# Kernel tuning notes

Hardware: AMD Instinct MI355X
Metric: run time of the kernel (lower is better)

Reference implementation:

```python
import jax, jax.numpy as jnp
import numpy as np

H, E, V, F, P, B = 512, 512, 10000, 1280, 196, 32
SOS = 1

def setup_inputs() -> dict:
    key = jax.random.key(0)
    ks = jax.random.split(key, 24)
    s = 0.02
    return {
        "feature_outputs": jax.random.normal(ks[0], (B, P, F), jnp.float32),
        "caption": jax.random.randint(ks[1], (B, 80), 0, V),
        "max_caption": 80,
        "embedding": jax.random.normal(ks[2], (V, E), jnp.float32) * s,
        "W1_w": jax.random.normal(ks[3], (H, H), jnp.float32) * s,
        "W1_b": jnp.full((H,), 0.01, jnp.float32),
        "W2_w": jax.random.normal(ks[4], (H, F), jnp.float32) * s,
        "W2_b": jnp.full((H,), 0.01, jnp.float32),
        "Va_w": jax.random.normal(ks[5], (1, H), jnp.float32) * s,
        "Va_b": jnp.full((1,), 0.01, jnp.float32),
        "lstm_Wih": jax.random.normal(ks[6], (4 * H, E + F), jnp.float32) * s,
        "lstm_Whh": jax.random.normal(ks[7], (4 * H, H), jnp.float32) * s,
        "lstm_bih": jnp.zeros((4 * H,), jnp.float32),
        "lstm_bhh": jnp.zeros((4 * H,), jnp.float32),
        "out_w": jax.random.normal(ks[8], (V, H), jnp.float32) * s,
        "out_b": jnp.full((V,), 0.01, jnp.float32),
        "init_h_w": jax.random.normal(ks[9], (H, F), jnp.float32) * s,
        "init_h_b": jnp.full((H,), 0.01, jnp.float32),
        "init_c_w": jax.random.normal(ks[10], (H, F), jnp.float32) * s,
        "init_c_b": jnp.full((H,), 0.01, jnp.float32),
        "gate_w": jax.random.normal(ks[11], (F, H), jnp.float32) * s,
        "gate_b": jnp.full((F,), 0.01, jnp.float32),
    }


def reference(feature_outputs, caption, max_caption, embedding,
              W1_w, W1_b, W2_w, W2_b, Va_w, Va_b,
              lstm_Wih, lstm_Whh, lstm_bih, lstm_bhh,
              out_w, out_b, init_h_w, init_h_b, init_c_w, init_c_b,
              gate_w, gate_b):
    steps = int(max_caption)
    bsz = caption.shape[0]
    mean_enc = feature_outputs.mean(axis=1)                       # [B,F]
    h0 = mean_enc @ init_h_w.T + init_h_b                         # [B,H]
    c0 = mean_enc @ init_c_w.T + init_c_b                         # [B,H]
    # W2(keys) is constant across steps -> hoist out of the loop
    enc_proj = jnp.einsum('bpf,hf->bph', feature_outputs, W2_w) + W2_b  # [B,P,H]
    inp0 = jnp.broadcast_to(embedding[SOS], (bsz, embedding.shape[1]))  # [B,E]

    def step(carry, _):
        h, c, inp = carry
        # Bahdanau attention
        hid = h @ W1_w.T + W1_b                                   # [B,H]
        scores = (jax.nn.relu(hid[:, None, :] + enc_proj) @ Va_w[0] + Va_b[0])  # [B,P]
        weights = jax.nn.softmax(scores, axis=1)
        context = jnp.einsum('bpf,bp->bf', feature_outputs, weights)  # [B,F]
        gate = jax.nn.sigmoid(h @ gate_w.T + gate_b)              # [B,F]
        context = context * gate
        # LSTMCell (torch gate order: i, f, g, o)
        x = jnp.concatenate([inp, context], axis=1)               # [B,E+F]
        gates = x @ lstm_Wih.T + lstm_bih + h @ lstm_Whh.T + lstm_bhh
        i_g, f_g, g_g, o_g = jnp.split(gates, 4, axis=1)
        c_new = jax.nn.sigmoid(f_g) * c + jax.nn.sigmoid(i_g) * jnp.tanh(g_g)
        h_new = jax.nn.sigmoid(o_g) * jnp.tanh(c_new)
        logits = h_new @ out_w.T + out_b                          # [B,V] (dropout = eval identity)
        nxt = embedding[jnp.argmax(logits, axis=-1)]              # greedy decode
        return (h_new, c_new, nxt), (logits, weights)

    (h, c, _), (outs, attns) = jax.lax.scan(step, (h0, c0, inp0), None, length=steps)
    decoder_outputs = jnp.transpose(outs, (1, 0, 2))              # [B,T,V]
    attentions = jnp.transpose(attns, (1, 0, 2))                  # [B,T,P]
    return decoder_outputs, (h, c), attentions
```

## Files before the change

### kernel.cpp

```cpp
#include <hip/hip_runtime.h>
#include <hip/hip_cooperative_groups.h>
#include <math.h>

#define RI __restrict__

namespace {

constexpr int Hn=512, En=512, Vn=10000, Fn=1280, Pn=196, Bn=32, Tn=80;
constexpr int G4 = 2048, KX = 1792;
constexpr int NCAT = 13888;
constexpr int NVT = 157;
constexpr int J_GATE = 512, J_XP = 1792, J_LOG = 3840;
constexpr int NBLK = 256;
constexpr int XROW = 140;

constexpr long O_ENC  = 0;
constexpr long O_W2T  = O_ENC  + (long)Bn*Pn*Hn;
constexpr long O_WCAT = O_W2T  + (long)Fn*Hn;
constexpr long O_WIHT = O_WCAT + (long)Hn*NCAT;
constexpr long O_C    = O_WIHT + (long)KX*G4;
constexpr long O_HT   = O_C    + (long)Bn*Hn;
constexpr long O_HID  = O_HT   + (long)Hn*Bn;
constexpr long O_GT   = O_HID  + (long)Bn*Hn;
constexpr long O_XPT  = O_GT   + (long)Bn*Fn;
constexpr long O_XT   = O_XPT  + (long)G4*Bn;
constexpr long O_PMV  = O_XT   + (long)Bn*KX;
constexpr long O_PMI  = O_PMV  + (long)Bn*NVT;
constexpr long O_SVAL = O_PMI  + (long)Bn*NVT;
constexpr long O_SEL  = O_SVAL + (long)Bn*Pn;
constexpr long O_CNT  = O_SEL  + 64;
constexpr long O_IHCT  = O_ENC;
constexpr long O_MEANT = O_ENC + (long)Fn*1024;

__device__ __forceinline__ float sigm(float x){ return 1.0f/(1.0f+expf(-x)); }
__device__ __forceinline__ void fma4(float4& a, const float4 x, const float w){
  a.x += w*x.x; a.y += w*x.y; a.z += w*x.z; a.w += w*x.w;
}
__device__ __forceinline__ float ldc(const float* p){
  return __hip_atomic_load(p, __ATOMIC_RELAXED, __HIP_MEMORY_SCOPE_AGENT);
}
__device__ __forceinline__ void stc(float* p, float v){
  __hip_atomic_store(p, v, __ATOMIC_RELAXED, __HIP_MEMORY_SCOPE_AGENT);
}
__device__ __forceinline__ int ldci(const int* p){
  return __hip_atomic_load(p, __ATOMIC_RELAXED, __HIP_MEMORY_SCOPE_AGENT);
}
__device__ __forceinline__ void stci(int* p, int v){
  __hip_atomic_store(p, v, __ATOMIC_RELAXED, __HIP_MEMORY_SCOPE_AGENT);
}
__device__ __forceinline__ float2 ldc2(const float* p){
  union { unsigned long long u; float2 f; } c;
  c.u = __hip_atomic_load((const unsigned long long*)p,
                          __ATOMIC_RELAXED, __HIP_MEMORY_SCOPE_AGENT);
  return c.f;
}

__device__ __forceinline__ void gbar(unsigned* cnt, unsigned target){
  __syncthreads();
  if (threadIdx.x == 0){
    __hip_atomic_fetch_add(cnt, 1u, __ATOMIC_RELAXED, __HIP_MEMORY_SCOPE_AGENT);
    while (__hip_atomic_load(cnt, __ATOMIC_RELAXED, __HIP_MEMORY_SCOPE_AGENT) < target)
      __builtin_amdgcn_s_sleep(2);
  }
  __syncthreads();
}

__global__ __launch_bounds__(256) void k_tr_s(const float* RI src, float* RI dst,
                                              int R, int C, int S){
  __shared__ float t[32][33];
  int tc0 = blockIdx.x*32, tr0 = blockIdx.y*32;
  int lx = threadIdx.x & 31, ly = threadIdx.x >> 5;
  for (int i = ly; i < 32; i += 8){
    int r = tr0 + i, c = tc0 + lx;
    t[i][lx] = (r < R && c < C) ? src[(long)r*C + c] : 0.f;
  }
  __syncthreads();
  for (int i = ly; i < 32; i += 8){
    int c = tc0 + i, r = tr0 + lx;
    if (c < C && r < R) dst[(long)c*S + r] = t[lx][i];
  }
}

__global__ __launch_bounds__(256) void k_tr_wih(const float* RI src, float* RI ws){
  __shared__ float t[32][33];
  int tk0 = blockIdx.x*32, tj0 = blockIdx.y*32;
  int lx = threadIdx.x & 31, ly = threadIdx.x >> 5;
  for (int i = ly; i < 32; i += 8){
    int j = tj0 + i, k = tk0 + lx;
    t[i][lx] = src[(long)j*KX + k];
  }
  __syncthreads();
  for (int i = ly; i < 32; i += 8){
    int k = tk0 + i, j = tj0 + lx;
    int pc = ((j & 511) << 2) | (j >> 9);
    ws[O_WIHT + ((long)(pc >> 3)*KX + k)*8 + (pc & 7)] = t[lx][i];
  }
}

__global__ __launch_bounds__(256) void k_mean(const float* RI feat, float* RI ws){
  int blk = blockIdx.x;
  int b = blk / 5, ft = blk % 5;
  int f = ft*256 + threadIdx.x;
  float s = 0.f;
  const float* fp = feat + (long)b*Pn*Fn + f;
  for (int p = 0; p < Pn; ++p) s += fp[(long)p*Fn];
  ws[O_MEANT + (long)f*Bn + b] = s * (1.0f/Pn);
}

__global__ __launch_bounds__(512) void k_h0c0(const float* RI ihb, const float* RI icb,
                                              float* RI ws){
  int tid = threadIdx.x;
  int jl = tid & 63, bq = tid >> 6;
  int j = blockIdx.x*64 + jl;
  const float* wp = ws + O_IHCT + j;
  const float* xp = ws + O_MEANT + bq*4;
  float4 acc = make_float4(0,0,0,0);
  for (int k = 0; k < Fn; ++k){
    float w = wp[(long)k*1024];
    float4 x = *(const float4*)(xp + (long)k*Bn);
    fma4(acc, x, w);
  }
  float va[4] = {acc.x, acc.y, acc.z, acc.w};
  if (j < Hn){
    float bias = ihb[j];
    #pragma unroll
    for (int m = 0; m < 4; ++m)
      ws[O_HT + (long)j*Bn + (bq*4+m)] = va[m] + bias;
  } else {
    int j2 = j - Hn;
    float bias = icb[j2];
    #pragma unroll
    for (int m = 0; m < 4; ++m)
      ws[O_C + (long)(bq*4+m)*Hn + j2] = va[m] + bias;
  }
}

__global__ __launch_bounds__(512) void k_encproj(const float* RI feat, const float* RI w2b,
                                                 float* RI ws){
  __shared__ __align__(16) float xs[64*65];
  const int blk = blockIdx.x;
  const int rt = blk >> 2, ct = blk & 3;
  const int r0 = rt*64, j0 = ct*128;
  const int tid = threadIdx.x;
  const int jq = tid & 31, rg = tid >> 5;
  const int rw = tid >> 3, kc = (tid & 7)*8;
  const float* w2t = ws + O_W2T + j0 + jq*4;
  float4 a0 = make_float4(0,0,0,0), a1 = a0, a2 = a0, a3 = a0;
  for (int k0 = 0; k0 < Fn; k0 += 64){
    __syncthreads();
    {
      const float* fp = feat + (long)(r0+rw)*Fn + k0 + kc;
      float4 v0 = *(const float4*)(fp);
      float4 v1 = *(const float4*)(fp + 4);
      float* xr = xs + rw*65 + kc;
      xr[0]=v0.x; xr[1]=v0.y; xr[2]=v0.z; xr[3]=v0.w;
      xr[4]=v1.x; xr[5]=v1.y; xr[6]=v1.z; xr[7]=v1.w;
    }
    __syncthreads();
    #pragma unroll 4
    for (int kk = 0; kk < 64; ++kk){
      float4 w = *(const float4*)(w2t + (long)(k0+kk)*Hn);
      const float* xp = xs + (rg*4)*65 + kk;
      fma4(a0, w, xp[0]);
      fma4(a1, w, xp[65]);
      fma4(a2, w, xp[130]);
      fma4(a3, w, xp[195]);
    }
  }
  float4 b4 = *(const float4*)(w2b + j0 + jq*4);
  float4 out[4] = {a0,a1,a2,a3};
  #pragma unroll
  for (int m = 0; m < 4; ++m){
    long r = r0 + rg*4 + m;
    float4 o = out[m];
    o.x += b4.x; o.y += b4.y; o.z += b4.z; o.w += b4.w;
    *(float4*)(ws + O_ENC + r*Hn + j0 + jq*4) = o;
  }
}

__global__ __launch_bounds__(512) void k_decode(
    const float* RI feat, const float* RI emb, const float* RI vaw, const float* RI vab,
    const float* RI w1b, const float* RI gb, const float* RI bih, const float* RI bhh,
    const float* RI outb, float* RI ws, float* RI dout)
{
  __shared__ __align__(16) float wlds[32768];
  __shared__ __align__(16) float sbuf[4608];
  const int blk = blockIdx.x, tid = threadIdx.x;
  const int jl = tid & 63, bq = tid >> 6;
  unsigned* cnt = (unsigned*)(ws + O_CNT);

  if (blk < 217){
    const float* wg = ws + O_WCAT + blk*64;
    for (int idx = tid; idx < 512*64; idx += 512){
      int k = idx >> 6, j = idx & 63;
      wlds[idx] = wg[(long)k*NCAT + j];
    }
  }
  __syncthreads();

  for (int t = 0; t <= Tn; ++t){
    bool p1act;
    if (t == Tn)      p1act = (blk >= 60 && blk < 217);
    else if (t == 0)  p1act = (blk < 60);
    else              p1act = (blk < 217);
    if (p1act){
      float4 acc = make_float4(0,0,0,0);
      float2 pre0 = ldc2(ws + O_HT + tid*2);
      float2 pre1 = ldc2(ws + O_HT + 1024 + tid*2);
      for (int c8 = 0; c8 < 8; ++c8){
        __syncthreads();
        *(float2*)(sbuf + tid*2) = pre0;
        *(float2*)(sbuf + 1024 + tid*2) = pre1;
        __syncthreads();
        if (c8 < 7){
          pre0 = ldc2(ws + O_HT + (long)(c8+1)*2048 + tid*2);
          pre1 = ldc2(ws + O_HT + (long)(c8+1)*2048 + 1024 + tid*2);
        }
        #pragma unroll 8
        for (int kk = 0; kk < 64; ++kk){
          float w = wlds[(long)(c8*64 + kk)*64 + jl];
          float4 x = *(const float4*)(sbuf + kk*32 + bq*4);
          fma4(acc, x, w);
        }
      }
      __syncthreads();
      const int j = blk*64 + jl;
      if (blk < 8){
        float bias = w1b[j];
        stc(ws + O_HID + (long)(bq*4+0)*Hn + j, acc.x + bias);
        stc(ws + O_HID + (long)(bq*4+1)*Hn + j, acc.y + bias);
        stc(ws + O_HID + (long)(bq*4+2)*Hn + j, acc.z + bias);
        stc(ws + O_HID + (long)(bq*4+3)*Hn + j, acc.w + bias);
      } else if (blk < 28){
        int f = j - J_GATE;
        float bias = gb[f];
        stc(ws + O_GT + (long)(bq*4+0)*Fn + f, sigm(acc.x + bias));
        stc(ws + O_GT + (long)(bq*4+1)*Fn + f, sigm(acc.y + bias));
        stc(ws + O_GT + (long)(bq*4+2)*Fn + f, sigm(acc.z + bias));
        stc(ws + O_GT + (long)(bq*4+3)*Fn + f, sigm(acc.w + bias));
      } else if (blk < 60){
        int j2 = j - J_XP;
        float bias = bih[j2] + bhh[j2];
        sbuf[jl*33 + bq*4+0] = acc.x + bias;
        sbuf[jl*33 + bq*4+1] = acc.y + bias;
        sbuf[jl*33 + bq*4+2] = acc.z + bias;
        sbuf[jl*33 + bq*4+3] = acc.w + bias;
        __syncthreads();
        #pragma unroll
        for (int r = 0; r < 4; ++r){
          int idx = r*512 + tid;
          int row = idx >> 5, b = idx & 31;
          int j2r = (blk-28)*64 + row;
          int pc = ((j2r & 511) << 2) | (j2r >> 9);
          stc(ws + O_XPT + (long)pc*Bn + b, sbuf[row*33 + b]);
        }
      } else {
        int v = j - J_LOG;
        float lv[4];
        if (v < Vn){
          float bias = outb[v];
          lv[0]=acc.x+bias; lv[1]=acc.y+bias; lv[2]=acc.z+bias; lv[3]=acc.w+bias;
          #pragma unroll
          for (int m = 0; m < 4; ++m)
            dout[((long)(bq*4+m)*Tn + (t-1))*Vn + v] = lv[m];
        } else {
          lv[0]=lv[1]=lv[2]=lv[3]=-1e30f;
        }
        int tile = blk - 60;
        #pragma unroll
        for (int m = 0; m < 4; ++m){
          float bv = lv[m]; int bi = v;
          #pragma unroll
          for (int off = 32; off; off >>= 1){
            float ov = __shfl_down(bv, off, 64);
            int   oi = __shfl_down(bi, off, 64);
            if (ov > bv || (ov == bv && oi < bi)){ bv = ov; bi = oi; }
          }
          if (jl == 0){
            int b = bq*4 + m;
            stc (ws + O_PMV + (long)b*NVT + tile, bv);
            stci((int*)(ws + O_PMI) + (long)b*NVT + tile, bi);
          }
        }
      }
    }
    gbar(cnt, 256u*(t+1));
    if (t == Tn) break;

    if (blk < 224){
      const int b = blk & 31, part = blk >> 5;
      float* hid_s = sbuf;
      float* va_s  = sbuf + 512;
      float* sv    = sbuf + 1024;
      hid_s[tid] = ldc(ws + O_HID + (long)b*Hn + tid);
      va_s[tid]  = vaw[tid];
      __syncthreads();
      const int w = tid >> 6, l = tid & 63;
      const int p0 = part*28;
      const float* eb = ws + O_ENC + (long)b*Pn*Hn;
      #pragma unroll 2
      for (int p = p0 + w; p < p0 + 28; p += 8){
        const float* er = eb + (long)p*Hn;
        float4 e0 = *(const float4*)(er + l*4);
        float4 e1 = *(const float4*)(er + 256 + l*4);
        float4 h0 = *(const float4*)(hid_s + l*4);
        float4 h1 = *(const float4*)(hid_s + 256 + l*4);
        float4 v0 = *(const float4*)(va_s + l*4);
        float4 v1 = *(const float4*)(va_s + 256 + l*4);
        float s = fmaxf(h0.x+e0.x,0.f)*v0.x + fmaxf(h0.y+e0.y,0.f)*v0.y
                + fmaxf(h0.z+e0.z,0.f)*v0.z + fmaxf(h0.w+e0.w,0.f)*v0.w
                + fmaxf(h1.x+e1.x,0.f)*v1.x + fmaxf(h1.y+e1.y,0.f)*v1.y
                + fmaxf(h1.z+e1.z,0.f)*v1.z + fmaxf(h1.w+e1.w,0.f)*v1.w;
        #pragma unroll
        for (int off = 32; off; off >>= 1) s += __shfl_down(s, off, 64);
        if (l == 0) sv[p - p0] = s + vab[0];
      }
      __syncthreads();
      if (tid < 28) stc(ws + O_SVAL + (long)b*Pn + p0 + tid, sv[tid]);
    } else {
      const int b = blk - 224;
      if (t == 0){
        if (tid == 0) stci((int*)(ws + O_SEL) + b, 1);
      } else if (tid < 64){
        float bv = -1e30f; int bi = 0x7fffffff;
        for (int q = tid; q < NVT; q += 64){
          float cv = ldc(ws + O_PMV + (long)b*NVT + q);
          if (cv > bv){ bv = cv; bi = ldci((const int*)(ws + O_PMI) + (long)b*NVT + q); }
        }
        #pragma unroll
        for (int off = 32; off; off >>= 1){
          float ov = __shfl_down(bv, off, 64);
          int   oi = __shfl_down(bi, off, 64);
          if (ov > bv || (ov == bv && oi < bi)){ bv = ov; bi = oi; }
        }
        if (tid == 0) stci((int*)(ws + O_SEL) + b, bi);
      }
    }
    gbar(cnt + 32, 256u*(t+1));

    {
      const int b = blk & 31, fr = blk >> 5;
      const int f0 = fr*160;
      float* svl = sbuf;
      float* wts = sbuf + 208;
      if (tid < Pn) svl[tid] = ldc(ws + O_SVAL + (long)b*Pn + tid);
      if (tid == 0) ((int*)sbuf)[450] = ldci((const int*)(ws + O_SEL) + b);
      __syncthreads();
      if (tid < 64){
        float m = -1e30f;
        for (int p = tid; p < Pn; p += 64) m = fmaxf(m, svl[p]);
        #pragma unroll
        for (int off = 32; off; off >>= 1) m = fmaxf(m, __shfl_xor(m, off, 64));
        float sm = 0.f;
        for (int p = tid; p < Pn; p += 64) sm += expf(svl[p] - m);
        #pragma unroll
        for (int off = 32; off; off >>= 1) sm += __shfl_xor(sm, off, 64);
        if (tid == 0){ sbuf[448] = m; sbuf[449] = 1.0f/sm; }
      }
      __syncthreads();
      if (tid < Pn){
        float wv = expf(svl[tid] - sbuf[448]) * sbuf[449];
        wts[tid] = wv;
        if (fr == 0)
          dout[(long)Bn*Tn*Vn + 2L*Bn*Hn + ((long)b*Tn + t)*Pn + tid] = wv;
      }
      __syncthreads();
      const int pp = tid / 160, fl = tid - pp*160;
      float a = 0.f;
      if (tid < 480){
        const int p0 = pp*66, pn = (pp == 2) ? 64 : 66;
        const float* fp = feat + ((long)b*Pn + p0)*Fn + f0 + fl;
        const float* wl = wts + p0;
        float s0=0,s1=0,s2=0,s3=0,s4=0,s5=0,s6=0,s7=0;
        int p = 0;
        for (; p + 8 <= pn; p += 8){
          s0 += wl[p+0]*__builtin_nontemporal_load(fp + (long)(p+0)*Fn);
          s1 += wl[p+1]*__builtin_nontemporal_load(fp + (long)(p+1)*Fn);
          s2 += wl[p+2]*__builtin_nontemporal_load(fp + (long)(p+2)*Fn);
          s3 += wl[p+3]*__builtin_nontemporal_load(fp + (long)(p+3)*Fn);
          s4 += wl[p+4]*__builtin_nontemporal_load(fp + (long)(p+4)*Fn);
          s5 += wl[p+5]*__builtin_nontemporal_load(fp + (long)(p+5)*Fn);
          s6 += wl[p+6]*__builtin_nontemporal_load(fp + (long)(p+6)*Fn);
          s7 += wl[p+7]*__builtin_nontemporal_load(fp + (long)(p+7)*Fn);
        }
        for (; p < pn; ++p) s0 += wl[p]*__builtin_nontemporal_load(fp + (long)p*Fn);
        a = ((s0+s1)+(s2+s3)) + ((s4+s5)+(s6+s7));
        if (pp > 0) sbuf[512 + (pp-1)*160 + fl] = a;
      }
      __syncthreads();
      if (tid < 160){
        float tot = a + sbuf[512 + tid] + sbuf[672 + tid];
        int f = f0 + tid;
        tot *= ldc(ws + O_GT + (long)b*Fn + f);
        stc(ws + O_XT + (long)b*KX + En + f, tot);
      }
      if (fr == 0){
        int row = ((int*)sbuf)[450];
        stc(ws + O_XT + (long)b*KX + tid, emb[(long)row*En + tid]);
      }
    }
    gbar(cnt + 64, 256u*(t+1));

    {
      const int c = tid & 7, ks = tid >> 3;
      const int pc0 = blk*8;
      const float* wg = ws + O_WIHT + (long)blk*KX*8;
      float4 acc4[8];
      #pragma unroll
      for (int q = 0; q < 8; ++q) acc4[q] = make_float4(0,0,0,0);
      float2 pre[4];
      #pragma unroll
      for (int r = 0; r < 4; ++r){
        int flat = r*1024 + tid*2;
        pre[r] = ldc2(ws + O_XT + (long)(flat >> 7)*KX + (flat & 127));
      }
      for (int ch = 0; ch < 14; ++ch){
        __syncthreads();
        #pragma unroll
        for (int r = 0; r < 4; ++r){
          int flat = r*1024 + tid*2;
          int kl = flat & 127, b = flat >> 7;
          int sc = kl + ((kl >> 5) << 2);
          float* xd = sbuf + b*XROW;
          xd[sc] = pre[r].x; xd[sc+1] = pre[r].y;
        }
        __syncthreads();
        if (ch < 13){
          long k0n = (long)(ch+1)*128;
          #pragma unroll
          for (int r = 0; r < 4; ++r){
            int flat = r*1024 + tid*2;
            pre[r] = ldc2(ws + O_XT + (long)(flat >> 7)*KX + k0n + (flat & 127));
          }
        }
        const long kg0 = (long)ch*128;
        #pragma unroll
        for (int kk = 0; kk < 2; ++kk){
          int kl = ks*2 + kk;
          float w = wg[(kg0 + kl)*8 + c];
          int cs = kl + ((kl >> 5) << 2);
          const float* xq = sbuf + cs;
          #pragma unroll
          for (int q = 0; q < 8; ++q){
            const float* xb = xq + (q*4)*XROW;
            acc4[q].x += w * xb[0];
            acc4[q].y += w * xb[XROW];
            acc4[q].z += w * xb[2*XROW];
            acc4[q].w += w * xb[3*XROW];
          }
        }
      }
      #pragma unroll
      for (int off = 8; off <= 32; off <<= 1){
        #pragma unroll
        for (int q = 0; q < 8; ++q){
          acc4[q].x += __shfl_xor(acc4[q].x, off, 64);
          acc4[q].y += __shfl_xor(acc4[q].y, off, 64);
          acc4[q].z += __shfl_xor(acc4[q].z, off, 64);
          acc4[q].w += __shfl_xor(acc4[q].w, off, 64);
        }
      }
      __syncthreads();
      const int wv = tid >> 6, lane = tid & 63;
      if (lane < 8){
        float* rb = sbuf + (wv*8 + lane)*32;
        #pragma unroll
        for (int q = 0; q < 8; ++q) *(float4*)(rb + q*4) = acc4[q];
      }
      __syncthreads();
      if (tid < 256){
        int cc = tid >> 5, b = tid & 31;
        float s = 0.f;
        #pragma unroll
        for (int w2 = 0; w2 < 8; ++w2) s += sbuf[(w2*8 + cc)*32 + b];
        s += ldc(ws + O_XPT + (long)(pc0 + cc)*Bn + b);
        sbuf[2048 + cc*32 + b] = s;
      }
      __syncthreads();
      if (tid < 64){
        int il = tid >> 5, b = tid & 31;
        int i = blk*2 + il;
        float gi  = sbuf[2048 + (il*4+0)*32 + b];
        float gf  = sbuf[2048 + (il*4+1)*32 + b];
        float gg2 = sbuf[2048 + (il*4+2)*32 + b];
        float go  = sbuf[2048 + (il*4+3)*32 + b];
        float c_ = ws[O_C + (long)b*Hn + i];
        float cn = sigm(gf)*c_ + sigm(gi)*tanhf(gg2);
        float hn = sigm(go)*tanhf(cn);
        ws[O_C + (long)b*Hn + i] = cn;
        stc(ws + O_HT + (long)i*Bn + b, hn);
        if (t == Tn-1){
          dout[(long)Bn*Tn*Vn + (long)b*Hn + i] = hn;
          dout[(long)Bn*Tn*Vn + (long)Bn*Hn + (long)b*Hn + i] = cn;
        }
      }
    }
    gbar(cnt + 96, 256u*(t+1));
  }
}

}

extern "C" void kernel_launch(void* const* d_in, const int* in_sizes, int n_in,
                              void* d_out, int out_size, void* d_ws, size_t ws_size,
                              hipStream_t stream)
{
  (void)in_sizes; (void)n_in; (void)out_size; (void)ws_size;
  const float* feat = (const float*)d_in[0];
  const float* emb  = (const float*)d_in[3];
  const float* w1w  = (const float*)d_in[4];
  const float* w1b  = (const float*)d_in[5];
  const float* w2w  = (const float*)d_in[6];
  const float* w2b  = (const float*)d_in[7];
  const float* vaw  = (const float*)d_in[8];
  const float* vab  = (const float*)d_in[9];
  const float* wih  = (const float*)d_in[10];
  const float* whh  = (const float*)d_in[11];
  const float* bih  = (const float*)d_in[12];
  const float* bhh  = (const float*)d_in[13];
  const float* outw = (const float*)d_in[14];
  const float* outb = (const float*)d_in[15];
  const float* ihw  = (const float*)d_in[16];
  const float* ihb  = (const float*)d_in[17];
  const float* icw  = (const float*)d_in[18];
  const float* icb  = (const float*)d_in[19];
  const float* gw   = (const float*)d_in[20];
  const float* gb   = (const float*)d_in[21];
  float* ws  = (float*)d_ws;
  float* out = (float*)d_out;

  hipMemsetAsync((char*)d_ws + O_CNT*sizeof(float), 0, 512, stream);

  k_tr_s<<<dim3(40,16),  256, 0, stream>>>(ihw,  ws + O_IHCT,       Hn, Fn, 1024);
  k_tr_s<<<dim3(40,16),  256, 0, stream>>>(icw,  ws + O_IHCT + 512, Hn, Fn, 1024);
  k_mean<<<160, 256, 0, stream>>>(feat, ws);
  k_h0c0<<<16, 512, 0, stream>>>(ihb, icb, ws);
  k_tr_s<<<dim3(16,16),  256, 0, stream>>>(w1w,  ws + O_WCAT,          Hn, Hn, NCAT);
  k_tr_s<<<dim3(16,40),  256, 0, stream>>>(gw,   ws + O_WCAT + J_GATE, Fn, Hn, NCAT);
  k_tr_s<<<dim3(16,64),  256, 0, stream>>>(whh,  ws + O_WCAT + J_XP,   G4, Hn, NCAT);
  k_tr_s<<<dim3(16,313), 256, 0, stream>>>(outw, ws + O_WCAT + J_LOG,  Vn, Hn, NCAT);
  k_tr_wih<<<dim3(56,64), 256, 0, stream>>>(wih, ws);
  k_tr_s<<<dim3(40,16),  256, 0, stream>>>(w2w,  ws + O_W2T,           Hn, Fn, Hn);
  k_encproj<<<392, 512, 0, stream>>>(feat, w2b, ws);

  void* kargs[] = { (void*)&feat, (void*)&emb, (void*)&vaw, (void*)&vab,
                    (void*)&w1b, (void*)&gb, (void*)&bih, (void*)&bhh,
                    (void*)&outb, (void*)&ws, (void*)&out };
  hipLaunchCooperativeKernel((const void*)k_decode, dim3(NBLK), dim3(512),
                             kargs, 0, stream);
}
```

Before: 6.401 ms.

## Replace grid-wide barriers with per-role dataflow counters in decode loop

The four full-grid barriers per timestep are replaced by fine-grained counters, one per producer role (hidden, gate, xproj, logits, per-batch scores and selection, x-transposes, h). Each phase now waits only on the specific data it consumes. This lets blocks run ahead and overlap stages, for example attention starting as soon as the W1 hidden projection is done. Feature loads in the context reduction also switch from nontemporal to normal cached loads. The risk is memory-ordering hazards with relaxed atomics and more polling traffic on the counters.

New measurement: 5.624 ms. 12.1% less time.

```diff
diff --git a/kernel.cpp b/kernel.cpp
--- a/kernel.cpp
+++ b/kernel.cpp
@@ -54,13 +54,24 @@
                           __ATOMIC_RELAXED, __HIP_MEMORY_SCOPE_AGENT);
   return c.f;
 }
-
-__device__ __forceinline__ void gbar(unsigned* cnt, unsigned target){
+__device__ __forceinline__ unsigned ldcu(const unsigned* p){
+  return __hip_atomic_load(p, __ATOMIC_RELAXED, __HIP_MEMORY_SCOPE_AGENT);
+}
+__device__ __forceinline__ void incc(unsigned* p){
+  __hip_atomic_fetch_add(p, 1u, __ATOMIC_RELAXED, __HIP_MEMORY_SCOPE_AGENT);
+}
+
+__device__ __forceinline__ void w1(const unsigned* a, unsigned ta){
+  if (threadIdx.x == 0){
+    while (ldcu(a) < ta) __builtin_amdgcn_s_sleep(2);
+  }
   __syncthreads();
+}
+__device__ __forceinline__ void w3(const unsigned* a, unsigned ta,
+                                   const unsigned* b, unsigned tb,
+                                   const unsigned* c, unsigned tc){
   if (threadIdx.x == 0){
-    __hip_atomic_fetch_add(cnt, 1u, __ATOMIC_RELAXED, __HIP_MEMORY_SCOPE_AGENT);
-    while (__hip_atomic_load(cnt, __ATOMIC_RELAXED, __HIP_MEMORY_SCOPE_AGENT) < target)
-      __builtin_amdgcn_s_sleep(2);
+    while (ldcu(a) < ta || ldcu(b) < tb || ldcu(c) < tc) __builtin_amdgcn_s_sleep(2);
   }
   __syncthreads();
 }
@@ -188,6 +199,15 @@
   const int blk = blockIdx.x, tid = threadIdx.x;
   const int jl = tid & 63, bq = tid >> 6;
   unsigned* cnt = (unsigned*)(ws + O_CNT);
+  unsigned* C_H   = cnt + 0;
+  unsigned* C_P1  = cnt + 32;
+  unsigned* C_HID = cnt + 64;
+  unsigned* C_GT  = cnt + 96;
+  unsigned* C_XP  = cnt + 128;
+  unsigned* C_LOG = cnt + 160;
+  unsigned* C_XT  = cnt + 192;
+  #define C_SC(b)  (cnt + 256 + (b)*8)
+  #define C_SEL(b) (cnt + 512 + (b)*8)
 
   if (blk < 217){
     const float* wg = ws + O_WCAT + blk*64;
@@ -199,96 +219,102 @@
   __syncthreads();
 
   for (int t = 0; t <= Tn; ++t){
-    bool p1act;
-    if (t == Tn)      p1act = (blk >= 60 && blk < 217);
-    else if (t == 0)  p1act = (blk < 60);
-    else              p1act = (blk < 217);
-    if (p1act){
-      float4 acc = make_float4(0,0,0,0);
-      float2 pre0 = ldc2(ws + O_HT + tid*2);
-      float2 pre1 = ldc2(ws + O_HT + 1024 + tid*2);
-      for (int c8 = 0; c8 < 8; ++c8){
+    if (blk < 217){
+      if (t > 0) w1(C_H, 256u*t);
+      bool p1act = (t == Tn) ? (blk >= 60) : !(t == 0 && blk >= 60);
+      if (p1act){
+        float4 acc = make_float4(0,0,0,0);
+        float2 pre0 = ldc2(ws + O_HT + tid*2);
+        float2 pre1 = ldc2(ws + O_HT + 1024 + tid*2);
+        for (int c8 = 0; c8 < 8; ++c8){
+          __syncthreads();
+          *(float2*)(sbuf + tid*2) = pre0;
+          *(float2*)(sbuf + 1024 + tid*2) = pre1;
+          __syncthreads();
+          if (c8 < 7){
+            pre0 = ldc2(ws + O_HT + (long)(c8+1)*2048 + tid*2);
+            pre1 = ldc2(ws + O_HT + (long)(c8+1)*2048 + 1024 + tid*2);
+          }
+          #pragma unroll 8
+          for (int kk = 0; kk < 64; ++kk){
+            float w = wlds[(long)(c8*64 + kk)*64 + jl];
+            float4 x = *(const float4*)(sbuf + kk*32 + bq*4);
+            fma4(acc, x, w);
+          }
+        }
         __syncthreads();
-        *(float2*)(sbuf + tid*2) = pre0;
-        *(float2*)(sbuf + 1024 + tid*2) = pre1;
-        __syncthreads();
-        if (c8 < 7){
-          pre0 = ldc2(ws + O_HT + (long)(c8+1)*2048 + tid*2);
-          pre1 = ldc2(ws + O_HT + (long)(c8+1)*2048 + 1024 + tid*2);
-        }
-        #pragma unroll 8
-        for (int kk = 0; kk < 64; ++kk){
-          float w = wlds[(long)(c8*64 + kk)*64 + jl];
-          float4 x = *(const float4*)(sbuf + kk*32 + bq*4);
-          fma4(acc, x, w);
-        }
-      }
-      __syncthreads();
-      const int j = blk*64 + jl;
-      if (blk < 8){
-        float bias = w1b[j];
-        stc(ws + O_HID + (long)(bq*4+0)*Hn + j, acc.x + bias);
-        stc(ws + O_HID + (long)(bq*4+1)*Hn + j, acc.y + bias);
-        stc(ws + O_HID + (long)(bq*4+2)*Hn + j, acc.z + bias);
-        stc(ws + O_HID + (long)(bq*4+3)*Hn + j, acc.w + bias);
-      } else if (blk < 28){
-        int f = j - J_GATE;
-        float bias = gb[f];
-        stc(ws + O_GT + (long)(bq*4+0)*Fn + f, sigm(acc.x + bias));
-        stc(ws + O_GT + (long)(bq*4+1)*Fn + f, sigm(acc.y + bias));
-        stc(ws + O_GT + (long)(bq*4+2)*Fn + f, sigm(acc.z + bias));
-        stc(ws + O_GT + (long)(bq*4+3)*Fn + f, sigm(acc.w + bias));
-      } else if (blk < 60){
-        int j2 = j - J_XP;
-        float bias = bih[j2] + bhh[j2];
-        sbuf[jl*33 + bq*4+0] = acc.x + bias;
-        sbuf[jl*33 + bq*4+1] = acc.y + bias;
-        sbuf[jl*33 + bq*4+2] = acc.z + bias;
-        sbuf[jl*33 + bq*4+3] = acc.w + bias;
-        __syncthreads();
-        #pragma unroll
-        for (int r = 0; r < 4; ++r){
-          int idx = r*512 + tid;
-          int row = idx >> 5, b = idx & 31;
-          int j2r = (blk-28)*64 + row;
-          int pc = ((j2r & 511) << 2) | (j2r >> 9);
-          stc(ws + O_XPT + (long)pc*Bn + b, sbuf[row*33 + b]);
-        }
-      } else {
-        int v = j - J_LOG;
-        float lv[4];
-        if (v < Vn){
-          float bias = outb[v];
-          lv[0]=acc.x+bias; lv[1]=acc.y+bias; lv[2]=acc.z+bias; lv[3]=acc.w+bias;
+        const int j = blk*64 + jl;
+        if (blk < 8){
+          float bias = w1b[j];
+          stc(ws + O_HID + (long)(bq*4+0)*Hn + j, acc.x + bias);
+          stc(ws + O_HID + (long)(bq*4+1)*Hn + j, acc.y + bias);
+          stc(ws + O_HID + (long)(bq*4+2)*Hn + j, acc.z + bias);
+          stc(ws + O_HID + (long)(bq*4+3)*Hn + j, acc.w + bias);
+        } else if (blk < 28){
+          int f = j - J_GATE;
+          float bias = gb[f];
+          stc(ws + O_GT + (long)(bq*4+0)*Fn + f, sigm(acc.x + bias));
+          stc(ws + O_GT + (long)(bq*4+1)*Fn + f, sigm(acc.y + bias));
+          stc(ws + O_GT + (long)(bq*4+2)*Fn + f, sigm(acc.z + bias));
+          stc(ws + O_GT + (long)(bq*4+3)*Fn + f, sigm(acc.w + bias));
+        } else if (blk < 60){
+          int j2 = j - J_XP;
+          float bias = bih[j2] + bhh[j2];
+          sbuf[jl*33 + bq*4+0] = acc.x + bias;
+          sbuf[jl*33 + bq*4+1] = acc.y + bias;
+          sbuf[jl*33 + bq*4+2] = acc.z + bias;
+          sbuf[jl*33 + bq*4+3] = acc.w + bias;
+          __syncthreads();
           #pragma unroll
-          for (int m = 0; m < 4; ++m)
-            dout[((long)(bq*4+m)*Tn + (t-1))*Vn + v] = lv[m];
+          for (int r = 0; r < 4; ++r){
+            int idx = r*512 + tid;
+            int row = idx >> 5, b = idx & 31;
+            int j2r = (blk-28)*64 + row;
+            int pc = ((j2r & 511) << 2) | (j2r >> 9);
+            stc(ws + O_XPT + (long)pc*Bn + b, sbuf[row*33 + b]);
+          }
         } else {
-          lv[0]=lv[1]=lv[2]=lv[3]=-1e30f;
-        }
-        int tile = blk - 60;
-        #pragma unroll
-        for (int m = 0; m < 4; ++m){
-          float bv = lv[m]; int bi = v;
+          int v = j - J_LOG;
+          float lv[4];
+          if (v < Vn){
+            float bias = outb[v];
+            lv[0]=acc.x+bias; lv[1]=acc.y+bias; lv[2]=acc.z+bias; lv[3]=acc.w+bias;
+            #pragma unroll
+            for (int m = 0; m < 4; ++m)
+              dout[((long)(bq*4+m)*Tn + (t-1))*Vn + v] = lv[m];
+          } else {
+            lv[0]=lv[1]=lv[2]=lv[3]=-1e30f;
+          }
+          int tile = blk - 60;
           #pragma unroll
-          for (int off = 32; off; off >>= 1){
-            float ov = __shfl_down(bv, off, 64);
-            int   oi = __shfl_down(bi, off, 64);
-            if (ov > bv || (ov == bv && oi < bi)){ bv = ov; bi = oi; }
-          }
-          if (jl == 0){
-            int b = bq*4 + m;
-            stc (ws + O_PMV + (long)b*NVT + tile, bv);
-            stci((int*)(ws + O_PMI) + (long)b*NVT + tile, bi);
-          }
-        }
-      }
-    }
-    gbar(cnt, 256u*(t+1));
+          for (int m = 0; m < 4; ++m){
+            float bv = lv[m]; int bi = v;
+            #pragma unroll
+            for (int off = 32; off; off >>= 1){
+              float ov = __shfl_down(bv, off, 64);
+              int   oi = __shfl_down(bi, off, 64);
+              if (ov > bv || (ov == bv && oi < bi)){ bv = ov; bi = oi; }
+            }
+            if (jl == 0){
+              int b = bq*4 + m;
+              stc (ws + O_PMV + (long)b*NVT + tile, bv);
+              stci((int*)(ws + O_PMI) + (long)b*NVT + tile, bi);
+            }
+          }
+        }
+      }
+      __syncthreads();
+      if (tid == 0){
+        unsigned* role = (blk < 8) ? C_HID : (blk < 28) ? C_GT
+                       : (blk < 60) ? C_XP : C_LOG;
+        incc(role); incc(C_P1);
+      }
+    }
     if (t == Tn) break;
 
     if (blk < 224){
       const int b = blk & 31, part = blk >> 5;
+      w1(C_HID, 8u*(t+1));
       float* hid_s = sbuf;
       float* va_s  = sbuf + 512;
       float* sv    = sbuf + 1024;
@@ -317,8 +343,11 @@
       }
       __syncthreads();
       if (tid < 28) stc(ws + O_SVAL + (long)b*Pn + p0 + tid, sv[tid]);
+      __syncthreads();
+      if (tid == 0) incc(C_SC(b));
     } else {
       const int b = blk - 224;
+      w1(C_LOG, 157u*(t+1));
       if (t == 0){
         if (tid == 0) stci((int*)(ws + O_SEL) + b, 1);
       } else if (tid < 64){
@@ -335,12 +364,14 @@
         }
         if (tid == 0) stci((int*)(ws + O_SEL) + b, bi);
       }
-    }
-    gbar(cnt + 32, 256u*(t+1));
+      __syncthreads();
+      if (tid == 0) incc(C_SEL(b));
+    }
 
     {
       const int b = blk & 31, fr = blk >> 5;
       const int f0 = fr*160;
+      w3(C_SC(b), 7u*(t+1), C_SEL(b), (unsigned)(t+1), C_GT, 20u*(t+1));
       float* svl = sbuf;
       float* wts = sbuf + 208;
       if (tid < Pn) svl[tid] = ldc(ws + O_SVAL + (long)b*Pn + tid);
@@ -374,16 +405,16 @@
         float s0=0,s1=0,s2=0,s3=0,s4=0,s5=0,s6=0,s7=0;
         int p = 0;
         for (; p + 8 <= pn; p += 8){
-          s0 += wl[p+0]*__builtin_nontemporal_load(fp + (long)(p+0)*Fn);
-          s1 += wl[p+1]*__builtin_nontemporal_load(fp + (long)(p+1)*Fn);
-          s2 += wl[p+2]*__builtin_nontemporal_load(fp + (long)(p+2)*Fn);
-          s3 += wl[p+3]*__builtin_nontemporal_load(fp + (long)(p+3)*Fn);
-          s4 += wl[p+4]*__builtin_nontemporal_load(fp + (long)(p+4)*Fn);
-          s5 += wl[p+5]*__builtin_nontemporal_load(fp + (long)(p+5)*Fn);
-          s6 += wl[p+6]*__builtin_nontemporal_load(fp + (long)(p+6)*Fn);
-          s7 += wl[p+7]*__builtin_nontemporal_load(fp + (long)(p+7)*Fn);
-        }
-        for (; p < pn; ++p) s0 += wl[p]*__builtin_nontemporal_load(fp + (long)p*Fn);
+          s0 += wl[p+0]*fp[(long)(p+0)*Fn];
+          s1 += wl[p+1]*fp[(long)(p+1)*Fn];
+          s2 += wl[p+2]*fp[(long)(p+2)*Fn];
+          s3 += wl[p+3]*fp[(long)(p+3)*Fn];
+          s4 += wl[p+4]*fp[(long)(p+4)*Fn];
+          s5 += wl[p+5]*fp[(long)(p+5)*Fn];
+          s6 += wl[p+6]*fp[(long)(p+6)*Fn];
+          s7 += wl[p+7]*fp[(long)(p+7)*Fn];
+        }
+        for (; p < pn; ++p) s0 += wl[p]*fp[(long)p*Fn];
         a = ((s0+s1)+(s2+s3)) + ((s4+s5)+(s6+s7));
         if (pp > 0) sbuf[512 + (pp-1)*160 + fl] = a;
       }
@@ -398,10 +429,12 @@
         int row = ((int*)sbuf)[450];
         stc(ws + O_XT + (long)b*KX + tid, emb[(long)row*En + tid]);
       }
-    }
-    gbar(cnt + 64, 256u*(t+1));
+      __syncthreads();
+      if (tid == 0) incc(C_XT);
+    }
 
     {
+      w3(C_XT, 256u*(t+1), C_XP, 32u*(t+1), C_P1, 217u*(t+1));
       const int c = tid & 7, ks = tid >> 3;
       const int pc0 = blk*8;
       const float* wg = ws + O_WIHT + (long)blk*KX*8;
@@ -494,9 +527,12 @@
           dout[(long)Bn*Tn*Vn + (long)Bn*Hn + (long)b*Hn + i] = cn;
         }
       }
-    }
-    gbar(cnt + 96, 256u*(t+1));
-  }
+      __syncthreads();
+      if (tid == 0) incc(C_H);
+    }
+  }
+  #undef C_SC
+  #undef C_SEL
 }
 
 }
@@ -529,7 +565,7 @@
   float* ws  = (float*)d_ws;
   float* out = (float*)d_out;
 
-  hipMemsetAsync((char*)d_ws + O_CNT*sizeof(float), 0, 512, stream);
+  hipMemsetAsync((char*)d_ws + O_CNT*sizeof(float), 0, 4096, stream);
 
   k_tr_s<<<dim3(40,16),  256, 0, stream>>>(ihw,  ws + O_IHCT,       Hn, Fn, 1024);
   k_tr_s<<<dim3(40,16),  256, 0, stream>>>(icw,  ws + O_IHCT + 512, Hn, Fn, 1024);
```
